# Optimization experiments

Measured on AMD Instinct MI355X. Metric: run time of the kernel, lower is better.

Reference implementation:

```python
import jax, jax.numpy as jnp
import numpy as np

B, H, N, D = 8, 12, 1024, 64
SCALE = 1.0 / float(np.sqrt(D))  # 0.125; torch forward default is 1.0 but 1/sqrt(d) is the production value
EPS = 1e-06


def setup_inputs() -> dict:
    key = jax.random.key(0)
    kq, kk, kv = jax.random.split(key, 3)
    q = jax.random.normal(kq, (B, H, N, D), dtype=jnp.float32)
    k = jax.random.normal(kk, (B, H, N, D), dtype=jnp.float32)
    v = jax.random.normal(kv, (B, H, N, D), dtype=jnp.float32)
    # Parameter init per L2Q.__init__: alpha=0.125, beta=0.5, gamma=1/n_tokens
    alpha = jnp.full((H, 1, 1), 0.125, dtype=jnp.float32)
    beta = jnp.full((H, 1, 1), 0.5, dtype=jnp.float32)
    gamma = jnp.full((H, 1, 1), 1.0 / N, dtype=jnp.float32)
    return {"q": q, "k": k, "v": v, "alpha": alpha, "beta": beta, "gamma": gamma}


def reference(q, k, v, alpha, beta, gamma):
    # logits: (B, H, N, N)
    logits = jnp.einsum("bhnd,bhmd->bhnm", q, k) * SCALE
    # per-head quadratic polynomial, then ReLU; params (H,1,1) broadcast over (B,H,N,N)
    attn = jax.nn.relu(alpha * logits * logits + beta * logits + gamma)
    attn = attn / (jnp.sum(attn, axis=-1, keepdims=True) + EPS)
    return jnp.einsum("bhnm,bhmd->bhnd", attn, v)
```

## Files before the change

### kernel.cpp

```cpp
#include <hip/hip_runtime.h>
#include <hip/hip_bf16.h>

typedef __attribute__((ext_vector_type(8))) short bf16x8;
typedef __attribute__((ext_vector_type(4))) float f32x4;

#define MFMA16(a, b, c) __builtin_amdgcn_mfma_f32_16x16x32_bf16(a, b, c, 0, 0, 0)

static constexpr int kH = 12;
static constexpr int kN = 1024;
static constexpr int kD = 64;
static constexpr int kBH = 96;
static constexpr int kND = kN * kD;
static constexpr int kTiles = kN / 32;
static constexpr float kScale = 0.125f;
static constexpr float kEps = 1e-6f;
static constexpr long kTensorElems = (long)kBH * kND;
static constexpr long kWsNeeded = 2 * kTensorElems * 2;

__device__ __forceinline__ unsigned bfbits(float x) {
    union { __hip_bfloat16 h; unsigned short u; } c;
    c.h = __float2bfloat16(x);
    return (unsigned)c.u;
}
__device__ __forceinline__ unsigned pack2_rne(float a, float b) {
    return bfbits(a) | (bfbits(b) << 16);
}
__device__ __forceinline__ unsigned pack2_rhu(float lo, float hi) {
    unsigned a = __builtin_bit_cast(unsigned, lo) + 0x8000u;
    unsigned b = __builtin_bit_cast(unsigned, hi) + 0x8000u;
    return __builtin_amdgcn_perm(b, a, 0x07060302u);
}
__device__ __forceinline__ void gl_lds16(const void* g, void* l) {
    __builtin_amdgcn_global_load_lds(
        (const __attribute__((address_space(1))) void*)g,
        (__attribute__((address_space(3))) void*)l, 16, 0, 0);
}

__global__ __launch_bounds__(256, 2) void prep(
    const float* __restrict__ k, const float* __restrict__ v,
    unsigned* __restrict__ kbf, unsigned* __restrict__ vtb)
{
    static constexpr int TS = 68;
    __shared__ float T32[64 * TS];
    const int bid = blockIdx.x;
    const int bh = bid >> 4, nt = bid & 15;
    const int t = threadIdx.x;

    const float* kp = k + (long)bh * kND + (long)nt * 64 * kD;
    unsigned* ko = kbf + ((long)bh * kND + (long)nt * 64 * kD) / 2;
#pragma unroll
    for (int r = 0; r < 4; ++r) {
        const int f4 = t + 256 * r;
        const float4 f = ((const float4*)kp)[f4];
        uint2 u;
        u.x = pack2_rne(f.x, f.y);
        u.y = pack2_rne(f.z, f.w);
        *(uint2*)&ko[f4 * 2] = u;
    }

    const float* vp = v + (long)bh * kND + (long)nt * 64 * kD;
#pragma unroll
    for (int r = 0; r < 4; ++r) {
        const int f4 = t + 256 * r;
        const int n = f4 >> 4, d4 = f4 & 15;
        const float4 f = *(const float4*)(vp + (long)n * kD + 4 * d4);
        *(float4*)&T32[n * TS + 4 * d4] = f;
    }
    __syncthreads();
    const int d = t >> 2, c = t & 3;
    unsigned u[8];
#pragma unroll
    for (int j = 0; j < 8; ++j) {
        const int key = c * 16 + 2 * j;
        u[j] = pack2_rne(T32[key * TS + d], T32[(key + 1) * TS + d]);
    }
    unsigned* dst = vtb + (long)bh * (kND / 2) + (long)d * (kN / 2) + nt * 32 + c * 8;
    *(uint4*)(dst)     = *(uint4*)&u[0];
    *(uint4*)(dst + 4) = *(uint4*)&u[4];
}

__global__ __launch_bounds__(256, 5) void l2q_main(
    const float* __restrict__ q,
    const unsigned short* __restrict__ kbf, const unsigned short* __restrict__ vtbf,
    const float* __restrict__ alpha, const float* __restrict__ beta, const float* __restrict__ gamma,
    float* __restrict__ out)
{
    __shared__ __align__(16) unsigned Ks[2][1024];
    __shared__ __align__(16) unsigned Vs[2][1024];
    __shared__ __align__(16) unsigned Pu[4][512];

    const int bid  = blockIdx.x;
    const int xcd  = bid & 7;
    const int s    = bid >> 3;
    const int bh   = xcd * 12 + (s % 12);
    const int qt   = s / 12;
    const int h    = bh % kH;
    const int t    = threadIdx.x;
    const int wave = t >> 6;
    const int lane = t & 63;
    const int quad = lane >> 4;
    const int l15  = lane & 15;

    const float al = alpha[h] * (kScale * kScale);
    const float be = beta[h] * kScale;
    const float ga = gamma[h];

    const float* qp = q + (long)bh * kND;
    const unsigned short* kp = kbf + (long)bh * kND;
    const unsigned short* vp = vtbf + (long)bh * kND;

    bf16x8 qa[2][2];
#pragma unroll
    for (int qb = 0; qb < 2; ++qb) {
        const int row = qt * 128 + wave * 32 + qb * 16 + l15;
#pragma unroll
        for (int kc = 0; kc < 2; ++kc) {
            const float* src = qp + (long)row * kD + kc * 32 + quad * 8;
            const float4 f0 = *(const float4*)(src);
            const float4 f1 = *(const float4*)(src + 4);
            uint4 u;
            u.x = pack2_rne(f0.x, f0.y);
            u.y = pack2_rne(f0.z, f0.w);
            u.z = pack2_rne(f1.x, f1.y);
            u.w = pack2_rne(f1.z, f1.w);
            qa[qb][kc] = __builtin_bit_cast(bf16x8, u);
        }
    }

    f32x4 oacc[2][4];
#pragma unroll
    for (int qb = 0; qb < 2; ++qb)
#pragma unroll
        for (int db = 0; db < 4; ++db)
            oacc[qb][db] = (f32x4){0.f, 0.f, 0.f, 0.f};
    f32x4 dsv[2] = {(f32x4){0.f,0.f,0.f,0.f}, (f32x4){0.f,0.f,0.f,0.f}};

    const int krow = wave * 8 + (lane >> 3);
    const int kgl  = (((lane & 7) ^ (krow & 7))) * 8;
    const int vrow = wave * 16 + (lane >> 2);
    const int vgl  = (((lane & 3) ^ (vrow & 3))) * 8;
    auto stageKV = [&](int buf, int tile) {
        const int k0 = tile * 32;
        gl_lds16(kp + (long)(k0 + krow) * kD + kgl, &Ks[buf][wave * 256]);
        gl_lds16(vp + (long)vrow * kN + k0 + vgl,   &Vs[buf][wave * 256]);
    };

    stageKV(0, 0);
    unsigned* Pw = Pu[wave];
    const int sw3 = l15 & 3, sw7 = l15 & 7;

    for (int tile = 0; tile < kTiles; ++tile) {
        const int buf = tile & 1;
        __syncthreads();
        if (tile + 1 < kTiles) stageKV(buf ^ 1, tile + 1);

        const unsigned* Kb = Ks[buf];
        const unsigned* Vb = Vs[buf];

        f32x4 st[2][2];
#pragma unroll
        for (int qb = 0; qb < 2; ++qb)
#pragma unroll
            for (int kb = 0; kb < 2; ++kb)
                st[qb][kb] = (f32x4){0.f, 0.f, 0.f, 0.f};
#pragma unroll
        for (int kb = 0; kb < 2; ++kb) {
            const int row = (kb * 16 + l15) * 32;
            bf16x8 kf0 = *(const bf16x8*)&Kb[row + ((quad ^ sw7) << 2)];
            bf16x8 kf1 = *(const bf16x8*)&Kb[row + (((4 + quad) ^ sw7) << 2)];
#pragma unroll
            for (int qb = 0; qb < 2; ++qb) {
                st[qb][kb] = MFMA16(kf0, qa[qb][0], st[qb][kb]);
                st[qb][kb] = MFMA16(kf1, qa[qb][1], st[qb][kb]);
            }
        }

#pragma unroll
        for (int qb = 0; qb < 2; ++qb) {
            const int pbase = (qb * 16 + l15) * 16;
#pragma unroll
            for (int kb = 0; kb < 2; ++kb) {
                f32x4 sfr = st[qb][kb];
                f32x4 w = sfr * al + be;
                w = w * sfr + ga;
                w[0] = fmaxf(w[0], 0.f); w[1] = fmaxf(w[1], 0.f);
                w[2] = fmaxf(w[2], 0.f); w[3] = fmaxf(w[3], 0.f);
                dsv[qb] += w;
                uint2 pk2;
                pk2.x = pack2_rhu(w[0], w[1]);
                pk2.y = pack2_rhu(w[2], w[3]);
                const int gr = kb * 2 + (quad >> 1);
                *(uint2*)&Pw[pbase + ((gr ^ sw3) << 2) + (quad & 1) * 2] = pk2;
            }
        }
        __asm__ __volatile__("" ::: "memory");

        bf16x8 pf[2];
        pf[0] = *(const bf16x8*)&Pw[(l15)      * 16 + ((quad ^ sw3) << 2)];
        pf[1] = *(const bf16x8*)&Pw[(16 + l15) * 16 + ((quad ^ sw3) << 2)];
#pragma unroll
        for (int db = 0; db < 4; ++db) {
            bf16x8 vf = *(const bf16x8*)&Vb[(db * 16 + l15) * 16 + ((quad ^ sw3) << 2)];
            oacc[0][db] = MFMA16(pf[0], vf, oacc[0][db]);
            oacc[1][db] = MFMA16(pf[1], vf, oacc[1][db]);
        }
        __asm__ __volatile__("" ::: "memory");
    }

    float dr[2];
#pragma unroll
    for (int qb = 0; qb < 2; ++qb) {
        float d = dsv[qb][0] + dsv[qb][1] + dsv[qb][2] + dsv[qb][3];
        d += __shfl_xor(d, 16);
        d += __shfl_xor(d, 32);
        dr[qb] = 1.0f / (d + kEps);
    }

    const long obase = (long)bh * kND;
#pragma unroll
    for (int qb = 0; qb < 2; ++qb)
#pragma unroll
        for (int i = 0; i < 4; ++i) {
            const float rr = __shfl(dr[qb], quad * 4 + i);
            const int row = qt * 128 + wave * 32 + qb * 16 + quad * 4 + i;
#pragma unroll
            for (int db = 0; db < 4; ++db)
                out[obase + (long)row * kD + db * 16 + l15] = oacc[qb][db][i] * rr;
        }
}

static constexpr int KSU = 36;
static constexpr int VSU = 36;
static constexpr int PSU = 36;

__global__ __launch_bounds__(256, 3) void l2q_attn_fb(
    const float* __restrict__ q, const float* __restrict__ k, const float* __restrict__ v,
    const float* __restrict__ alpha, const float* __restrict__ beta, const float* __restrict__ gamma,
    float* __restrict__ out)
{
    __shared__ __align__(16) unsigned KsU[64 * KSU];
    __shared__ __align__(16) unsigned VtU[64 * VSU];
    __shared__ __align__(16) unsigned PU[128 * PSU];

    const int bid  = blockIdx.x;
    const int bh   = bid >> 3;
    const int qt   = bid & 7;
    const int h    = bh % kH;
    const int t    = threadIdx.x;
    const int wave = t >> 6;
    const int lane = t & 63;
    const int quad = lane >> 4;
    const int l15  = lane & 15;

    const float al = alpha[h], be = beta[h], ga = gamma[h];

    const long base = (long)bh * kN * kD;
    const float* qp = q + base;
    const float* kp = k + base;
    const float* vp = v + base;

    bf16x8 qa[2][2];
#pragma unroll
    for (int rb = 0; rb < 2; ++rb) {
        const int row = qt * 128 + wave * 32 + rb * 16 + l15;
#pragma unroll
        for (int kc = 0; kc < 2; ++kc) {
            const float* src = qp + (long)row * kD + kc * 32 + quad * 8;
            const float4 f0 = *(const float4*)(src);
            const float4 f1 = *(const float4*)(src + 4);
            uint4 u;
            u.x = pack2_rne(f0.x, f0.y);
            u.y = pack2_rne(f0.z, f0.w);
            u.z = pack2_rne(f1.x, f1.y);
            u.w = pack2_rne(f1.z, f1.w);
            qa[rb][kc] = __builtin_bit_cast(bf16x8, u);
        }
    }

    f32x4 oacc[2][4];
#pragma unroll
    for (int rb = 0; rb < 2; ++rb)
#pragma unroll
        for (int db = 0; db < 4; ++db)
            oacc[rb][db] = (f32x4){0.f, 0.f, 0.f, 0.f};

    float dsum[2][4] = {{0.f, 0.f, 0.f, 0.f}, {0.f, 0.f, 0.f, 0.f}};
    unsigned* Pw = &PU[wave * 32 * PSU];

    for (int tile = 0; tile < 16; ++tile) {
        __syncthreads();
        const int k0 = tile * 64;
#pragma unroll
        for (int r = 0; r < 4; ++r) {
            const int f4 = t + 256 * r;
            const int n = f4 >> 4, d4 = f4 & 15;
            const float4 kg = *(const float4*)(kp + (long)(k0 + n) * kD + 4 * d4);
            uint2 pk;
            pk.x = pack2_rne(kg.x, kg.y);
            pk.y = pack2_rne(kg.z, kg.w);
            *(uint2*)&KsU[n * KSU + 2 * d4] = pk;
        }
#pragma unroll
        for (int r = 0; r < 2; ++r) {
            const int u = t + 256 * r;
            const int key2 = u & 31, d4 = u >> 5;
            const float* s0 = vp + (long)(k0 + 2 * key2) * kD + 4 * d4;
            const float4 va = *(const float4*)(s0);
            const float4 vb = *(const float4*)(s0 + kD);
            VtU[(4 * d4 + 0) * VSU + key2] = pack2_rne(va.x, vb.x);
            VtU[(4 * d4 + 1) * VSU + key2] = pack2_rne(va.y, vb.y);
            VtU[(4 * d4 + 2) * VSU + key2] = pack2_rne(va.z, vb.z);
            VtU[(4 * d4 + 3) * VSU + key2] = pack2_rne(va.w, vb.w);
        }
        __syncthreads();

        f32x4 s[2][4];
#pragma unroll
        for (int rb = 0; rb < 2; ++rb)
#pragma unroll
            for (int nb = 0; nb < 4; ++nb)
                s[rb][nb] = (f32x4){0.f, 0.f, 0.f, 0.f};
#pragma unroll
        for (int nb = 0; nb < 4; ++nb) {
            bf16x8 kb0 = *(const bf16x8*)&KsU[(nb * 16 + l15) * KSU + 4 * quad];
            bf16x8 kb1 = *(const bf16x8*)&KsU[(nb * 16 + l15) * KSU + 16 + 4 * quad];
#pragma unroll
            for (int rb = 0; rb < 2; ++rb) {
                s[rb][nb] = MFMA16(qa[rb][0], kb0, s[rb][nb]);
                s[rb][nb] = MFMA16(qa[rb][1], kb1, s[rb][nb]);
            }
        }

        const bool ev = (lane & 1) == 0;
#pragma unroll
        for (int rb = 0; rb < 2; ++rb) {
#pragma unroll
            for (int nb = 0; nb < 4; ++nb) {
                float w0, w1, w2, w3;
                {
                    float l0 = s[rb][nb][0] * kScale;
                    float l1 = s[rb][nb][1] * kScale;
                    float l2 = s[rb][nb][2] * kScale;
                    float l3 = s[rb][nb][3] * kScale;
                    w0 = fmaxf(fmaf(fmaf(al, l0, be), l0, ga), 0.f);
                    w1 = fmaxf(fmaf(fmaf(al, l1, be), l1, ga), 0.f);
                    w2 = fmaxf(fmaf(fmaf(al, l2, be), l2, ga), 0.f);
                    w3 = fmaxf(fmaf(fmaf(al, l3, be), l3, ga), 0.f);
                }
                dsum[rb][0] += w0; dsum[rb][1] += w1;
                dsum[rb][2] += w2; dsum[rb][3] += w3;

                const float o0 = __shfl_xor(w0, 1);
                const float o1 = __shfl_xor(w1, 1);
                const float o2 = __shfl_xor(w2, 1);
                const float o3 = __shfl_xor(w3, 1);
                const unsigned pa = ev ? pack2_rne(w0, o0) : pack2_rne(o2, w2);
                const unsigned pb = ev ? pack2_rne(w1, o1) : pack2_rne(o3, w3);
                const int r0 = ev ? 0 : 2;
                const int cu = (16 * nb + (l15 & ~1)) >> 1;
                const int rowb = rb * 16 + quad * 4 + r0;
                Pw[rowb * PSU + cu] = pa;
                Pw[(rowb + 1) * PSU + cu] = pb;
            }
        }

        bf16x8 pf[2][2];
#pragma unroll
        for (int rb = 0; rb < 2; ++rb)
#pragma unroll
            for (int kc = 0; kc < 2; ++kc)
                pf[rb][kc] = *(const bf16x8*)&Pw[(rb * 16 + l15) * PSU + 16 * kc + 4 * quad];
#pragma unroll
        for (int db = 0; db < 4; ++db) {
            bf16x8 vf0 = *(const bf16x8*)&VtU[(db * 16 + l15) * VSU + 4 * quad];
            bf16x8 vf1 = *(const bf16x8*)&VtU[(db * 16 + l15) * VSU + 16 + 4 * quad];
#pragma unroll
            for (int rb = 0; rb < 2; ++rb) {
                oacc[rb][db] = MFMA16(pf[rb][0], vf0, oacc[rb][db]);
                oacc[rb][db] = MFMA16(pf[rb][1], vf1, oacc[rb][db]);
            }
        }
    }

#pragma unroll
    for (int rb = 0; rb < 2; ++rb)
#pragma unroll
        for (int i = 0; i < 4; ++i) {
            float d = dsum[rb][i];
            d += __shfl_xor(d, 1);
            d += __shfl_xor(d, 2);
            d += __shfl_xor(d, 4);
            d += __shfl_xor(d, 8);
            dsum[rb][i] = 1.0f / (d + kEps);
        }

#pragma unroll
    for (int rb = 0; rb < 2; ++rb)
#pragma unroll
        for (int db = 0; db < 4; ++db)
#pragma unroll
            for (int i = 0; i < 4; ++i) {
                const int row = qt * 128 + wave * 32 + rb * 16 + quad * 4 + i;
                out[base + (long)row * kD + db * 16 + l15] = oacc[rb][db][i] * dsum[rb][i];
            }
}

extern "C" void kernel_launch(void* const* d_in, const int* in_sizes, int n_in,
                              void* d_out, int out_size, void* d_ws, size_t ws_size,
                              hipStream_t stream) {
    const float* q     = (const float*)d_in[0];
    const float* k     = (const float*)d_in[1];
    const float* v     = (const float*)d_in[2];
    const float* alpha = (const float*)d_in[3];
    const float* beta  = (const float*)d_in[4];
    const float* gamma = (const float*)d_in[5];
    float* out = (float*)d_out;

    if (ws_size < (size_t)kWsNeeded) {
        l2q_attn_fb<<<dim3(768), dim3(256), 0, stream>>>(q, k, v, alpha, beta, gamma, out);
        return;
    }

    unsigned* kbf = (unsigned*)d_ws;
    unsigned* vtb = kbf + kTensorElems / 2;

    prep<<<dim3(1536), dim3(256), 0, stream>>>(k, v, kbf, vtb);
    l2q_main<<<dim3(768), dim3(256), 0, stream>>>(
        q, (const unsigned short*)kbf, (const unsigned short*)vtb,
        alpha, beta, gamma, out);
}
```

Baseline: 157.9 us.

## Split key dimension across waves and halve q rows per block

Each block now handles 64 query rows with waves split two-by-two over query and key halves, processing 64-key tiles, and doubles the grid to 1536 blocks. Partial outputs and denominators from the two key halves are reduced through shared memory before the final write. The double-buffered K/V prefetch is replaced by a load-sync-compute pattern with two barriers per tile. The aim is more blocks for occupancy, at the cost of doubled K/V reads, lost load overlap and an extra epilogue reduction.

```diff
diff --git a/kernel.cpp b/kernel.cpp
--- a/kernel.cpp
+++ b/kernel.cpp
@@ -11,7 +11,6 @@
 static constexpr int kD = 64;
 static constexpr int kBH = 96;
 static constexpr int kND = kN * kD;
-static constexpr int kTiles = kN / 32;
 static constexpr float kScale = 0.125f;
 static constexpr float kEps = 1e-6f;
 static constexpr long kTensorElems = (long)kBH * kND;
@@ -85,21 +84,24 @@
     const float* __restrict__ alpha, const float* __restrict__ beta, const float* __restrict__ gamma,
     float* __restrict__ out)
 {
-    __shared__ __align__(16) unsigned Ks[2][1024];
-    __shared__ __align__(16) unsigned Vs[2][1024];
-    __shared__ __align__(16) unsigned Pu[4][512];
+    __shared__ __align__(16) unsigned SMEM[6656];
+    unsigned* Ks = SMEM;
+    unsigned* Vs = SMEM + 2048;
+    unsigned* Pu = SMEM + 4096;
 
     const int bid  = blockIdx.x;
     const int xcd  = bid & 7;
-    const int s    = bid >> 3;
-    const int bh   = xcd * 12 + (s % 12);
-    const int qt   = s / 12;
+    const int sIdx = bid >> 3;
+    const int bh   = xcd * 12 + (sIdx % 12);
+    const int qt   = sIdx / 12;
     const int h    = bh % kH;
     const int t    = threadIdx.x;
     const int wave = t >> 6;
     const int lane = t & 63;
     const int quad = lane >> 4;
     const int l15  = lane & 15;
+    const int ks   = wave & 1;
+    const int qs   = wave >> 1;
 
     const float al = alpha[h] * (kScale * kScale);
     const float be = beta[h] * kScale;
@@ -111,8 +113,8 @@
 
     bf16x8 qa[2][2];
 #pragma unroll
-    for (int qb = 0; qb < 2; ++qb) {
-        const int row = qt * 128 + wave * 32 + qb * 16 + l15;
+    for (int nb = 0; nb < 2; ++nb) {
+        const int row = qt * 64 + qs * 32 + nb * 16 + l15;
 #pragma unroll
         for (int kc = 0; kc < 2; ++kc) {
             const float* src = qp + (long)row * kD + kc * 32 + quad * 8;
@@ -123,7 +125,7 @@
             u.y = pack2_rne(f0.z, f0.w);
             u.z = pack2_rne(f1.x, f1.y);
             u.w = pack2_rne(f1.z, f1.w);
-            qa[qb][kc] = __builtin_bit_cast(bf16x8, u);
+            qa[nb][kc] = __builtin_bit_cast(bf16x8, u);
         }
     }
 
@@ -133,100 +135,123 @@
 #pragma unroll
         for (int db = 0; db < 4; ++db)
             oacc[qb][db] = (f32x4){0.f, 0.f, 0.f, 0.f};
-    f32x4 dsv[2] = {(f32x4){0.f,0.f,0.f,0.f}, (f32x4){0.f,0.f,0.f,0.f}};
-
-    const int krow = wave * 8 + (lane >> 3);
-    const int kgl  = (((lane & 7) ^ (krow & 7))) * 8;
-    const int vrow = wave * 16 + (lane >> 2);
-    const int vgl  = (((lane & 3) ^ (vrow & 3))) * 8;
-    auto stageKV = [&](int buf, int tile) {
-        const int k0 = tile * 32;
-        gl_lds16(kp + (long)(k0 + krow) * kD + kgl, &Ks[buf][wave * 256]);
-        gl_lds16(vp + (long)vrow * kN + k0 + vgl,   &Vs[buf][wave * 256]);
-    };
-
-    stageKV(0, 0);
-    unsigned* Pw = Pu[wave];
-    const int sw3 = l15 & 3, sw7 = l15 & 7;
-
-    for (int tile = 0; tile < kTiles; ++tile) {
-        const int buf = tile & 1;
+    float dsum[2] = {0.f, 0.f};
+
+    unsigned* Pw = Pu + wave * 640;
+    const int srow8 = lane >> 3;
+    const int g8    = lane & 7;
+    const int sw3   = l15 & 3;
+
+    for (int tile = 0; tile < 16; ++tile) {
         __syncthreads();
-        if (tile + 1 < kTiles) stageKV(buf ^ 1, tile + 1);
-
-        const unsigned* Kb = Ks[buf];
-        const unsigned* Vb = Vs[buf];
+        const int k0 = tile * 64;
+#pragma unroll
+        for (int c = 0; c < 2; ++c) {
+            const int r = (c * 4 + wave) * 8 + srow8;
+            gl_lds16(kp + (long)(k0 + r) * kD + (g8 ^ (r & 7)) * 8, &Ks[(c * 4 + wave) * 256]);
+            gl_lds16(vp + (long)r * kN + k0 + (g8 ^ (r & 7)) * 8, &Vs[(c * 4 + wave) * 256]);
+        }
+        __syncthreads();
 
         f32x4 st[2][2];
 #pragma unroll
-        for (int qb = 0; qb < 2; ++qb)
-#pragma unroll
-            for (int kb = 0; kb < 2; ++kb)
-                st[qb][kb] = (f32x4){0.f, 0.f, 0.f, 0.f};
+        for (int kb = 0; kb < 2; ++kb)
+#pragma unroll
+            for (int nb = 0; nb < 2; ++nb)
+                st[kb][nb] = (f32x4){0.f, 0.f, 0.f, 0.f};
 #pragma unroll
         for (int kb = 0; kb < 2; ++kb) {
-            const int row = (kb * 16 + l15) * 32;
-            bf16x8 kf0 = *(const bf16x8*)&Kb[row + ((quad ^ sw7) << 2)];
-            bf16x8 kf1 = *(const bf16x8*)&Kb[row + (((4 + quad) ^ sw7) << 2)];
-#pragma unroll
-            for (int qb = 0; qb < 2; ++qb) {
-                st[qb][kb] = MFMA16(kf0, qa[qb][0], st[qb][kb]);
-                st[qb][kb] = MFMA16(kf1, qa[qb][1], st[qb][kb]);
-            }
-        }
-
-#pragma unroll
-        for (int qb = 0; qb < 2; ++qb) {
-            const int pbase = (qb * 16 + l15) * 16;
+            const int krow = ks * 32 + kb * 16 + l15;
+            const int sw = krow & 7;
+            const int rbase = krow * 32;
+            bf16x8 kf0 = *(const bf16x8*)&Ks[rbase + ((quad ^ sw) << 2)];
+            bf16x8 kf1 = *(const bf16x8*)&Ks[rbase + (((4 + quad) ^ sw) << 2)];
+#pragma unroll
+            for (int nb = 0; nb < 2; ++nb) {
+                st[kb][nb] = MFMA16(kf0, qa[nb][0], st[kb][nb]);
+                st[kb][nb] = MFMA16(kf1, qa[nb][1], st[kb][nb]);
+            }
+        }
+
+#pragma unroll
+        for (int nb = 0; nb < 2; ++nb) {
+            const int pbase = (nb * 16 + l15) * 20;
+            float dadd = 0.f;
 #pragma unroll
             for (int kb = 0; kb < 2; ++kb) {
-                f32x4 sfr = st[qb][kb];
-                f32x4 w = sfr * al + be;
-                w = w * sfr + ga;
+                f32x4 sv = st[kb][nb];
+                f32x4 w = sv * al + be;
+                w = w * sv + ga;
                 w[0] = fmaxf(w[0], 0.f); w[1] = fmaxf(w[1], 0.f);
                 w[2] = fmaxf(w[2], 0.f); w[3] = fmaxf(w[3], 0.f);
-                dsv[qb] += w;
+                dadd += (w[0] + w[1]) + (w[2] + w[3]);
                 uint2 pk2;
                 pk2.x = pack2_rhu(w[0], w[1]);
                 pk2.y = pack2_rhu(w[2], w[3]);
-                const int gr = kb * 2 + (quad >> 1);
-                *(uint2*)&Pw[pbase + ((gr ^ sw3) << 2) + (quad & 1) * 2] = pk2;
-            }
+                const int g = kb * 2 + (quad >> 1);
+                *(uint2*)&Pw[pbase + ((g ^ sw3) << 2) + (quad & 1) * 2] = pk2;
+            }
+            dsum[nb] += dadd;
         }
         __asm__ __volatile__("" ::: "memory");
 
         bf16x8 pf[2];
-        pf[0] = *(const bf16x8*)&Pw[(l15)      * 16 + ((quad ^ sw3) << 2)];
-        pf[1] = *(const bf16x8*)&Pw[(16 + l15) * 16 + ((quad ^ sw3) << 2)];
+        pf[0] = *(const bf16x8*)&Pw[(l15)      * 20 + ((quad ^ sw3) << 2)];
+        pf[1] = *(const bf16x8*)&Pw[(16 + l15) * 20 + ((quad ^ sw3) << 2)];
 #pragma unroll
         for (int db = 0; db < 4; ++db) {
-            bf16x8 vf = *(const bf16x8*)&Vb[(db * 16 + l15) * 16 + ((quad ^ sw3) << 2)];
+            const int vrow = db * 16 + l15;
+            bf16x8 vf = *(const bf16x8*)&Vs[vrow * 32 + (((ks * 4 + quad) ^ (vrow & 7)) << 2)];
             oacc[0][db] = MFMA16(pf[0], vf, oacc[0][db]);
             oacc[1][db] = MFMA16(pf[1], vf, oacc[1][db]);
         }
         __asm__ __volatile__("" ::: "memory");
     }
 
-    float dr[2];
-#pragma unroll
-    for (int qb = 0; qb < 2; ++qb) {
-        float d = dsv[qb][0] + dsv[qb][1] + dsv[qb][2] + dsv[qb][3];
+    float* DredF = (float*)Pu;
+    float* O1 = (float*)(SMEM + qs * 2048);
+
+    float dred[2];
+#pragma unroll
+    for (int nb = 0; nb < 2; ++nb) {
+        float d = dsum[nb];
         d += __shfl_xor(d, 16);
         d += __shfl_xor(d, 32);
-        dr[qb] = 1.0f / (d + kEps);
-    }
-
-    const long obase = (long)bh * kND;
-#pragma unroll
-    for (int qb = 0; qb < 2; ++qb)
-#pragma unroll
-        for (int i = 0; i < 4; ++i) {
-            const float rr = __shfl(dr[qb], quad * 4 + i);
-            const int row = qt * 128 + wave * 32 + qb * 16 + quad * 4 + i;
+        dred[nb] = d;
+    }
+    __syncthreads();
+    if (quad == 0) {
+#pragma unroll
+        for (int nb = 0; nb < 2; ++nb)
+            DredF[(qs * 32 + nb * 16 + l15) * 2 + ks] = dred[nb];
+    }
+    if (ks == 1) {
+#pragma unroll
+        for (int qb = 0; qb < 2; ++qb)
 #pragma unroll
             for (int db = 0; db < 4; ++db)
-                out[obase + (long)row * kD + db * 16 + l15] = oacc[qb][db][i] * rr;
-        }
+#pragma unroll
+                for (int i = 0; i < 4; ++i)
+                    O1[(qb * 16 + quad * 4 + i) * 64 + db * 16 + l15] = oacc[qb][db][i];
+    }
+    __syncthreads();
+    if (ks == 0) {
+        const long obase = (long)bh * kND;
+#pragma unroll
+        for (int qb = 0; qb < 2; ++qb)
+#pragma unroll
+            for (int i = 0; i < 4; ++i) {
+                const int ql = qb * 16 + quad * 4 + i;
+                const float dd = DredF[(qs * 32 + ql) * 2 + 0] + DredF[(qs * 32 + ql) * 2 + 1];
+                const float inv = 1.0f / (dd + kEps);
+                const int row = qt * 64 + qs * 32 + ql;
+#pragma unroll
+                for (int db = 0; db < 4; ++db) {
+                    const float val = (oacc[qb][db][i] + O1[ql * 64 + db * 16 + l15]) * inv;
+                    out[obase + (long)row * kD + db * 16 + l15] = val;
+                }
+            }
+    }
 }
 
 static constexpr int KSU = 36;
@@ -425,7 +450,7 @@
     unsigned* vtb = kbf + kTensorElems / 2;
 
     prep<<<dim3(1536), dim3(256), 0, stream>>>(k, v, kbf, vtb);
-    l2q_main<<<dim3(768), dim3(256), 0, stream>>>(
+    l2q_main<<<dim3(1536), dim3(256), 0, stream>>>(
         q, (const unsigned short*)kbf, (const unsigned short*)vtb,
         alpha, beta, gamma, out);
 }
```

After: 188.5 us. 19.4% more time.

## Switch main attention kernel to 32x32x16 MFMA with register P exchange

Applied to the files above, without the earlier changes.

Rewrites the main loop to use 32x32x16 bf16 MFMAs in place of 16x16x32, computing S transposed so the polynomial weights can be repacked into A-operand fragments with cross-half-wave shuffles. This removes the per-wave LDS round trip for P. Key/value tiles are enlarged from 32 to 64 keys per iteration, which halves the number of barriers and doubles shared memory per block. Occupancy is lowered from 5 to 3 blocks per CU to fit the larger accumulators and buffers.

```diff
diff --git a/kernel.cpp b/kernel.cpp
--- a/kernel.cpp
+++ b/kernel.cpp
@@ -3,15 +3,16 @@
 
 typedef __attribute__((ext_vector_type(8))) short bf16x8;
 typedef __attribute__((ext_vector_type(4))) float f32x4;
+typedef __attribute__((ext_vector_type(16))) float f32x16;
 
 #define MFMA16(a, b, c) __builtin_amdgcn_mfma_f32_16x16x32_bf16(a, b, c, 0, 0, 0)
+#define MFMA32(a, b, c) __builtin_amdgcn_mfma_f32_32x32x16_bf16(a, b, c, 0, 0, 0)
 
 static constexpr int kH = 12;
 static constexpr int kN = 1024;
 static constexpr int kD = 64;
 static constexpr int kBH = 96;
 static constexpr int kND = kN * kD;
-static constexpr int kTiles = kN / 32;
 static constexpr float kScale = 0.125f;
 static constexpr float kEps = 1e-6f;
 static constexpr long kTensorElems = (long)kBH * kND;
@@ -79,27 +80,26 @@
     *(uint4*)(dst + 4) = *(uint4*)&u[4];
 }
 
-__global__ __launch_bounds__(256, 5) void l2q_main(
+__global__ __launch_bounds__(256, 3) void l2q_main(
     const float* __restrict__ q,
     const unsigned short* __restrict__ kbf, const unsigned short* __restrict__ vtbf,
     const float* __restrict__ alpha, const float* __restrict__ beta, const float* __restrict__ gamma,
     float* __restrict__ out)
 {
-    __shared__ __align__(16) unsigned Ks[2][1024];
-    __shared__ __align__(16) unsigned Vs[2][1024];
-    __shared__ __align__(16) unsigned Pu[4][512];
+    __shared__ __align__(16) unsigned Ks[2][2048];
+    __shared__ __align__(16) unsigned Vs[2][2048];
 
     const int bid  = blockIdx.x;
     const int xcd  = bid & 7;
-    const int s    = bid >> 3;
-    const int bh   = xcd * 12 + (s % 12);
-    const int qt   = s / 12;
+    const int sIdx = bid >> 3;
+    const int bh   = xcd * 12 + (sIdx % 12);
+    const int qt   = sIdx / 12;
     const int h    = bh % kH;
     const int t    = threadIdx.x;
     const int wave = t >> 6;
     const int lane = t & 63;
-    const int quad = lane >> 4;
-    const int l15  = lane & 15;
+    const int l31  = lane & 31;
+    const int hh   = lane >> 5;
 
     const float al = alpha[h] * (kScale * kScale);
     const float be = beta[h] * kScale;
@@ -109,124 +109,127 @@
     const unsigned short* kp = kbf + (long)bh * kND;
     const unsigned short* vp = vtbf + (long)bh * kND;
 
-    bf16x8 qa[2][2];
-#pragma unroll
-    for (int qb = 0; qb < 2; ++qb) {
-        const int row = qt * 128 + wave * 32 + qb * 16 + l15;
-#pragma unroll
-        for (int kc = 0; kc < 2; ++kc) {
-            const float* src = qp + (long)row * kD + kc * 32 + quad * 8;
-            const float4 f0 = *(const float4*)(src);
-            const float4 f1 = *(const float4*)(src + 4);
+    bf16x8 qbF[4];
+    {
+        const int qrow = qt * 128 + wave * 32 + l31;
+        const float* qsrc = qp + (long)qrow * kD;
+#pragma unroll
+        for (int s = 0; s < 4; ++s) {
+            const float4 f0 = *(const float4*)(qsrc + s * 16 + hh * 8);
+            const float4 f1 = *(const float4*)(qsrc + s * 16 + hh * 8 + 4);
             uint4 u;
             u.x = pack2_rne(f0.x, f0.y);
             u.y = pack2_rne(f0.z, f0.w);
             u.z = pack2_rne(f1.x, f1.y);
             u.w = pack2_rne(f1.z, f1.w);
-            qa[qb][kc] = __builtin_bit_cast(bf16x8, u);
-        }
-    }
-
-    f32x4 oacc[2][4];
-#pragma unroll
-    for (int qb = 0; qb < 2; ++qb)
-#pragma unroll
-        for (int db = 0; db < 4; ++db)
-            oacc[qb][db] = (f32x4){0.f, 0.f, 0.f, 0.f};
-    f32x4 dsv[2] = {(f32x4){0.f,0.f,0.f,0.f}, (f32x4){0.f,0.f,0.f,0.f}};
-
-    const int krow = wave * 8 + (lane >> 3);
-    const int kgl  = (((lane & 7) ^ (krow & 7))) * 8;
-    const int vrow = wave * 16 + (lane >> 2);
-    const int vgl  = (((lane & 3) ^ (vrow & 3))) * 8;
+            qbF[s] = __builtin_bit_cast(bf16x8, u);
+        }
+    }
+
+    f32x16 oacc[2];
+#pragma unroll
+    for (int db = 0; db < 2; ++db)
+#pragma unroll
+        for (int r = 0; r < 16; ++r)
+            oacc[db][r] = 0.f;
+    float dacc[4] = {0.f, 0.f, 0.f, 0.f};
+
+    const int srow8 = lane >> 3;
+    const int g8    = lane & 7;
     auto stageKV = [&](int buf, int tile) {
-        const int k0 = tile * 32;
-        gl_lds16(kp + (long)(k0 + krow) * kD + kgl, &Ks[buf][wave * 256]);
-        gl_lds16(vp + (long)vrow * kN + k0 + vgl,   &Vs[buf][wave * 256]);
+        const int k0 = tile * 64;
+#pragma unroll
+        for (int c = 0; c < 2; ++c) {
+            const int r = (c * 4 + wave) * 8 + srow8;
+            gl_lds16(kp + (long)(k0 + r) * kD + (g8 ^ srow8) * 8, &Ks[buf][(c * 4 + wave) * 256]);
+            gl_lds16(vp + (long)r * kN + k0 + (g8 ^ srow8) * 8, &Vs[buf][(c * 4 + wave) * 256]);
+        }
     };
 
     stageKV(0, 0);
-    unsigned* Pw = Pu[wave];
-    const int sw3 = l15 & 3, sw7 = l15 & 7;
-
-    for (int tile = 0; tile < kTiles; ++tile) {
+
+    for (int tile = 0; tile < 16; ++tile) {
         const int buf = tile & 1;
         __syncthreads();
-        if (tile + 1 < kTiles) stageKV(buf ^ 1, tile + 1);
+        if (tile + 1 < 16) stageKV(buf ^ 1, tile + 1);
 
         const unsigned* Kb = Ks[buf];
         const unsigned* Vb = Vs[buf];
 
-        f32x4 st[2][2];
-#pragma unroll
-        for (int qb = 0; qb < 2; ++qb)
-#pragma unroll
-            for (int kb = 0; kb < 2; ++kb)
-                st[qb][kb] = (f32x4){0.f, 0.f, 0.f, 0.f};
+        f32x16 st[2];
+#pragma unroll
+        for (int kb = 0; kb < 2; ++kb)
+#pragma unroll
+            for (int r = 0; r < 16; ++r)
+                st[kb][r] = 0.f;
+#pragma unroll
+        for (int s = 0; s < 4; ++s) {
+            const int g = (s << 1) | hh;
+#pragma unroll
+            for (int kb = 0; kb < 2; ++kb) {
+                const int row = kb * 32 + l31;
+                bf16x8 ka = *(const bf16x8*)&Kb[row * 32 + ((g ^ (row & 7)) << 2)];
+                st[kb] = MFMA32(ka, qbF[s], st[kb]);
+            }
+        }
+
+        unsigned u[2][8];
 #pragma unroll
         for (int kb = 0; kb < 2; ++kb) {
-            const int row = (kb * 16 + l15) * 32;
-            bf16x8 kf0 = *(const bf16x8*)&Kb[row + ((quad ^ sw7) << 2)];
-            bf16x8 kf1 = *(const bf16x8*)&Kb[row + (((4 + quad) ^ sw7) << 2)];
-#pragma unroll
-            for (int qb = 0; qb < 2; ++qb) {
-                st[qb][kb] = MFMA16(kf0, qa[qb][0], st[qb][kb]);
-                st[qb][kb] = MFMA16(kf1, qa[qb][1], st[qb][kb]);
-            }
-        }
-
-#pragma unroll
-        for (int qb = 0; qb < 2; ++qb) {
-            const int pbase = (qb * 16 + l15) * 16;
-#pragma unroll
-            for (int kb = 0; kb < 2; ++kb) {
-                f32x4 sfr = st[qb][kb];
-                f32x4 w = sfr * al + be;
-                w = w * sfr + ga;
-                w[0] = fmaxf(w[0], 0.f); w[1] = fmaxf(w[1], 0.f);
-                w[2] = fmaxf(w[2], 0.f); w[3] = fmaxf(w[3], 0.f);
-                dsv[qb] += w;
-                uint2 pk2;
-                pk2.x = pack2_rhu(w[0], w[1]);
-                pk2.y = pack2_rhu(w[2], w[3]);
-                const int gr = kb * 2 + (quad >> 1);
-                *(uint2*)&Pw[pbase + ((gr ^ sw3) << 2) + (quad & 1) * 2] = pk2;
-            }
-        }
-        __asm__ __volatile__("" ::: "memory");
-
-        bf16x8 pf[2];
-        pf[0] = *(const bf16x8*)&Pw[(l15)      * 16 + ((quad ^ sw3) << 2)];
-        pf[1] = *(const bf16x8*)&Pw[(16 + l15) * 16 + ((quad ^ sw3) << 2)];
-#pragma unroll
-        for (int db = 0; db < 4; ++db) {
-            bf16x8 vf = *(const bf16x8*)&Vb[(db * 16 + l15) * 16 + ((quad ^ sw3) << 2)];
-            oacc[0][db] = MFMA16(pf[0], vf, oacc[0][db]);
-            oacc[1][db] = MFMA16(pf[1], vf, oacc[1][db]);
-        }
-        __asm__ __volatile__("" ::: "memory");
-    }
-
-    float dr[2];
-#pragma unroll
-    for (int qb = 0; qb < 2; ++qb) {
-        float d = dsv[qb][0] + dsv[qb][1] + dsv[qb][2] + dsv[qb][3];
-        d += __shfl_xor(d, 16);
-        d += __shfl_xor(d, 32);
-        dr[qb] = 1.0f / (d + kEps);
-    }
+#pragma unroll
+            for (int p = 0; p < 8; ++p) {
+                const float s0 = st[kb][2 * p], s1 = st[kb][2 * p + 1];
+                const float w0 = fmaxf(fmaf(fmaf(al, s0, be), s0, ga), 0.f);
+                const float w1 = fmaxf(fmaf(fmaf(al, s1, be), s1, ga), 0.f);
+                dacc[p & 3] += w0 + w1;
+                u[kb][p] = pack2_rhu(w0, w1);
+            }
+        }
+
+        bf16x8 pa[4];
+#pragma unroll
+        for (int s = 0; s < 4; ++s) {
+            const int kb = s >> 1;
+            const int b = (s & 1) * 4;
+            const unsigned snd0 = hh ? u[kb][b + 0] : u[kb][b + 2];
+            const unsigned snd1 = hh ? u[kb][b + 1] : u[kb][b + 3];
+            const unsigned r0 = (unsigned)__shfl_xor((int)snd0, 32);
+            const unsigned r1 = (unsigned)__shfl_xor((int)snd1, 32);
+            uint4 fr;
+            fr.x = hh ? r0 : u[kb][b + 0];
+            fr.y = hh ? r1 : u[kb][b + 1];
+            fr.z = hh ? u[kb][b + 2] : r0;
+            fr.w = hh ? u[kb][b + 3] : r1;
+            pa[s] = __builtin_bit_cast(bf16x8, fr);
+        }
+
+#pragma unroll
+        for (int db = 0; db < 2; ++db) {
+            const int row = db * 32 + l31;
+            const int rb = row * 32;
+            const int rsw = row & 7;
+#pragma unroll
+            for (int s = 0; s < 4; ++s) {
+                bf16x8 vb = *(const bf16x8*)&Vb[rb + ((((s << 1) | hh) ^ rsw) << 2)];
+                oacc[db] = MFMA32(pa[s], vb, oacc[db]);
+            }
+        }
+    }
+
+    float d = (dacc[0] + dacc[1]) + (dacc[2] + dacc[3]);
+    d += __shfl_xor(d, 32);
+    const float inv = 1.0f / (d + kEps);
 
     const long obase = (long)bh * kND;
-#pragma unroll
-    for (int qb = 0; qb < 2; ++qb)
-#pragma unroll
-        for (int i = 0; i < 4; ++i) {
-            const float rr = __shfl(dr[qb], quad * 4 + i);
-            const int row = qt * 128 + wave * 32 + qb * 16 + quad * 4 + i;
-#pragma unroll
-            for (int db = 0; db < 4; ++db)
-                out[obase + (long)row * kD + db * 16 + l15] = oacc[qb][db][i] * rr;
-        }
+    const int rowbase = qt * 128 + wave * 32;
+#pragma unroll
+    for (int r = 0; r < 16; ++r) {
+        const int row32 = (r & 3) + 8 * (r >> 2) + 4 * hh;
+        const float iv = __shfl(inv, row32);
+        float* o = out + obase + (long)(rowbase + row32) * kD + l31;
+        o[0]  = oacc[0][r] * iv;
+        o[32] = oacc[1][r] * iv;
+    }
 }
 
 static constexpr int KSU = 36;
```

Result: faster. 151.0 us (-4.4%).
